# Kernel tuning notes

Hardware: AMD Instinct MI355X
Metric: run time of the kernel (lower is better)

## Reference

```python
import jax, jax.numpy as jnp
import numpy as np

N, K, R = 32768, 4096, 256

def setup_inputs() -> dict:
    key = jax.random.key(0)
    k1, k2, k3 = jax.random.split(key, 3)
    H = jax.random.normal(k1, (N, R), dtype=jnp.float32)
    L = jax.random.normal(k2, (K, R), dtype=jnp.float32)
    W_I = jax.random.normal(k3, (R, R), dtype=jnp.float32)
    return {"H": H, "L": L, "W_I": W_I}

def reference(H, L, W_I):
    # Q = W_I @ L^T : (r, k)
    Q = jnp.einsum('rs,ks->rk', W_I, L)
    # M_I = H @ Q : (n, k)
    M_I = jnp.einsum('nr,rk->nk', H, Q)
    A_I = jax.nn.softmax(M_I, axis=1)
    # C_I = A_I @ L : (n, r)
    C_I = jnp.einsum('nk,kr->nr', A_I, L)
    return (C_I, A_I)
```

## Files before the change

### kernel.cpp

```cpp
#include <hip/hip_runtime.h>
#include <hip/hip_bf16.h>
#include <math.h>
#include <stdint.h>

constexpr int N_ROWS = 32768;
constexpr int K_DIM  = 4096;
constexpr int R_DIM  = 256;
constexpr int KP     = 3 * R_DIM;

typedef __bf16 bf16x8 __attribute__((ext_vector_type(8)));
typedef float  f32x4  __attribute__((ext_vector_type(4)));
typedef unsigned short u16x8 __attribute__((ext_vector_type(8)));
typedef unsigned short u16x4 __attribute__((ext_vector_type(4)));

__device__ __forceinline__ unsigned short f2bf(float x) {
    unsigned u = __float_as_uint(x);
    u += 0x7fffu + ((u >> 16) & 1u);
    return (unsigned short)(u >> 16);
}
__device__ __forceinline__ float bf2f(unsigned short h) {
    return __uint_as_float((unsigned)h << 16);
}

__device__ __forceinline__ void gl2lds16(const void* gptr, void* lptr) {
    __builtin_amdgcn_global_load_lds(
        (const __attribute__((address_space(1))) unsigned int*)gptr,
        (__attribute__((address_space(3))) unsigned int*)lptr,
        16, 0, 0);
}

__global__ __launch_bounds__(256)
void gemm_mfma_nt(const unsigned short* __restrict__ A,
                  const unsigned short* __restrict__ B,
                  float* __restrict__ C, int M, int N, int Kc)
{
    __shared__ __align__(16) unsigned short As[128 * 32];
    __shared__ __align__(16) unsigned short Bs[128 * 32];

    const int tid  = threadIdx.x;
    const int wave = tid >> 6, lane = tid & 63;
    const int wm = wave >> 1, wn = wave & 1;
    const long m0 = (long)blockIdx.x * 128;
    const long n0 = (long)blockIdx.y * 128;

    f32x4 acc[4][4] = {};

    const int srow  = lane >> 2;
    const int skoff = (lane & 3) * 8;
    const int c0 = wave, c1 = wave + 4;
    const int kq = (lane >> 4) * 8;
    const int mr = lane & 15;

    for (int k0 = 0; k0 < Kc; k0 += 32) {
        gl2lds16(A + (m0 + c0 * 16 + srow) * (long)Kc + k0 + skoff, &As[c0 * 512]);
        gl2lds16(A + (m0 + c1 * 16 + srow) * (long)Kc + k0 + skoff, &As[c1 * 512]);
        gl2lds16(B + (n0 + c0 * 16 + srow) * (long)Kc + k0 + skoff, &Bs[c0 * 512]);
        gl2lds16(B + (n0 + c1 * 16 + srow) * (long)Kc + k0 + skoff, &Bs[c1 * 512]);
        __syncthreads();

        bf16x8 af[4], bfr[4];
#pragma unroll
        for (int t = 0; t < 4; ++t) {
            af[t]  = *(const bf16x8*)&As[(wm * 64 + t * 16 + mr) * 32 + kq];
            bfr[t] = *(const bf16x8*)&Bs[(wn * 64 + t * 16 + mr) * 32 + kq];
        }
#pragma unroll
        for (int i = 0; i < 4; ++i)
#pragma unroll
            for (int j = 0; j < 4; ++j)
                acc[i][j] = __builtin_amdgcn_mfma_f32_16x16x32_bf16(
                    af[i], bfr[j], acc[i][j], 0, 0, 0);
        __syncthreads();
    }

    const int col = lane & 15, rquad = (lane >> 4) * 4;
#pragma unroll
    for (int i = 0; i < 4; ++i) {
        const long mrow = m0 + wm * 64 + i * 16 + rquad;
#pragma unroll
        for (int j = 0; j < 4; ++j) {
            float* p = C + mrow * (long)N + n0 + wn * 64 + j * 16 + col;
#pragma unroll
            for (int r = 0; r < 4; ++r) p[(long)r * N] = acc[i][j][r];
        }
    }
}

__global__ __launch_bounds__(512)
void softmax_av(float* __restrict__ Mio,
                const unsigned short* __restrict__ LT,
                float* __restrict__ C)
{
    __shared__ __align__(16) unsigned short Bs[R_DIM * 64];
    __shared__ __align__(16) unsigned short As[64 * 64];
    __shared__ float sm_m[64], sm_inv[64];

    const int tid  = threadIdx.x;
    const int wave = tid >> 6, lane = tid & 63;
    const long m0 = (long)blockIdx.x * 64;

    for (int rr = 0; rr < 8; ++rr) {
        const int row = wave * 8 + rr;
        const float* rp = Mio + (m0 + row) * (long)K_DIM;
        float m = -3.4e38f, s = 0.f;
#pragma unroll
        for (int it = 0; it < 16; ++it) {
            float4 v = ((const float4*)rp)[lane + 64 * it];
            float cm = fmaxf(fmaxf(v.x, v.y), fmaxf(v.z, v.w));
            if (cm > m) { s *= __expf(m - cm); m = cm; }
            s += __expf(v.x - m) + __expf(v.y - m) +
                 __expf(v.z - m) + __expf(v.w - m);
        }
#pragma unroll
        for (int off = 1; off < 64; off <<= 1) {
            float om = __shfl_xor(m, off), os = __shfl_xor(s, off);
            float nm = fmaxf(m, om);
            s = s * __expf(m - nm) + os * __expf(om - nm);
            m = nm;
        }
        if (lane == 0) { sm_m[row] = m; sm_inv[row] = 1.f / s; }
    }
    __syncthreads();

    f32x4 acc[2][4] = {};
    const int wm = wave >> 2, wn = wave & 3;
    const int mr = lane & 15;
    const int kq16 = (lane >> 4) * 16;

    for (int k0 = 0; k0 < K_DIM; k0 += 64) {
#pragma unroll
        for (int q = 0; q < 4; ++q) {
            const int rbase = q * 64 + wave * 8;
            const int rloc  = rbase + (lane >> 3);
            const int phys  = (lane & 7) * 16;
            const int kbyte = phys ^ ((rloc & 7) << 4);
            gl2lds16((const char*)LT + (long)rloc * (K_DIM * 2) + (long)k0 * 2 + kbyte,
                     &Bs[rbase * 64]);
        }
#pragma unroll
        for (int p = 0; p < 2; ++p) {
            const int row = p * 32 + wave * 4 + (lane >> 4);
            const int col = (lane & 15) * 4;
            float* gp = Mio + (m0 + row) * (long)K_DIM + k0 + col;
            float4 v = *(const float4*)gp;
            const float mrow = sm_m[row], inv = sm_inv[row];
            float e0 = __expf(v.x - mrow), e1 = __expf(v.y - mrow);
            float e2 = __expf(v.z - mrow), e3 = __expf(v.w - mrow);
            *(float4*)gp = make_float4(e0 * inv, e1 * inv, e2 * inv, e3 * inv);
            u16x4 u;
            u[0] = f2bf(e0); u[1] = f2bf(e1); u[2] = f2bf(e2); u[3] = f2bf(e3);
            const int byte = (row * 128 + col * 2) ^ ((row & 7) << 4);
            *(u16x4*)((char*)As + byte) = u;
        }
        __syncthreads();

#pragma unroll
        for (int ks = 0; ks < 2; ++ks) {
            bf16x8 af[2], bfr[4];
#pragma unroll
            for (int t = 0; t < 2; ++t) {
                const int arow = wm * 32 + t * 16 + mr;
                const int ab = (arow * 128 + ks * 64 + kq16) ^ ((arow & 7) << 4);
                af[t] = *(const bf16x8*)((const char*)As + ab);
            }
#pragma unroll
            for (int t = 0; t < 4; ++t) {
                const int brow = wn * 64 + t * 16 + mr;
                const int bb = (brow * 128 + ks * 64 + kq16) ^ ((brow & 7) << 4);
                bfr[t] = *(const bf16x8*)((const char*)Bs + bb);
            }
#pragma unroll
            for (int i = 0; i < 2; ++i)
#pragma unroll
                for (int j = 0; j < 4; ++j)
                    acc[i][j] = __builtin_amdgcn_mfma_f32_16x16x32_bf16(
                        af[i], bfr[j], acc[i][j], 0, 0, 0);
        }
        __syncthreads();
    }

    const int col = lane & 15, rquad = (lane >> 4) * 4;
#pragma unroll
    for (int i = 0; i < 2; ++i) {
        const int lrow0 = wm * 32 + i * 16 + rquad;
#pragma unroll
        for (int j = 0; j < 4; ++j) {
            float* p = C + (m0 + lrow0) * (long)R_DIM + wn * 64 + j * 16 + col;
#pragma unroll
            for (int r = 0; r < 4; ++r)
                p[(long)r * R_DIM] = acc[i][j][r] * sm_inv[lrow0 + r];
        }
    }
}

__global__ __launch_bounds__(256)
void prep_B(const float* __restrict__ L, unsigned short* __restrict__ Bp)
{
    const long i = (long)blockIdx.x * 256 + threadIdx.x;
    const long k = i >> 8; const int r = (int)(i & 255);
    const float x = L[i];
    const unsigned short hi = f2bf(x);
    const unsigned short lo = f2bf(x - bf2f(hi));
    unsigned short* row = Bp + k * KP;
    row[r] = hi; row[R_DIM + r] = lo; row[2 * R_DIM + r] = hi;
}

__global__ __launch_bounds__(256)
void prep_LT(const float* __restrict__ L, unsigned short* __restrict__ LT)
{
    const long i = (long)blockIdx.x * 256 + threadIdx.x;
    const long r = i >> 12; const long k = i & 4095;
    LT[r * K_DIM + k] = f2bf(L[k * R_DIM + r]);
}

template<bool BT>
__global__ __launch_bounds__(256)
void gemm128(const float* __restrict__ A, const float* __restrict__ B,
             float* __restrict__ C, int M, int N, int Kc)
{
    __shared__ __align__(16) float Asl[16][132];
    __shared__ __align__(16) float Bsl[16][132];

    const int tid = threadIdx.x;
    const int tx = tid & 15, ty = tid >> 4;
    const long m0 = (long)blockIdx.x * 128;
    const long n0 = (long)blockIdx.y * 128;

    float acc[8][8];
#pragma unroll
    for (int i = 0; i < 8; ++i)
#pragma unroll
        for (int j = 0; j < 8; ++j) acc[i][j] = 0.f;

    for (int k0 = 0; k0 < Kc; k0 += 16) {
#pragma unroll
        for (int q = 0; q < 2; ++q) {
            int fi = tid + 256 * q, row = fi >> 2, col = (fi & 3) * 4;
            float4 v = *(const float4*)(A + (m0 + row) * (long)Kc + k0 + col);
            Asl[col + 0][row] = v.x; Asl[col + 1][row] = v.y;
            Asl[col + 2][row] = v.z; Asl[col + 3][row] = v.w;
        }
        if (BT) {
#pragma unroll
            for (int q = 0; q < 2; ++q) {
                int fi = tid + 256 * q, row = fi >> 2, col = (fi & 3) * 4;
                float4 v = *(const float4*)(B + (n0 + row) * (long)Kc + k0 + col);
                Bsl[col + 0][row] = v.x; Bsl[col + 1][row] = v.y;
                Bsl[col + 2][row] = v.z; Bsl[col + 3][row] = v.w;
            }
        } else {
#pragma unroll
            for (int q = 0; q < 2; ++q) {
                int fi = tid + 256 * q, row = fi >> 5, col = (fi & 31) * 4;
                float4 v = *(const float4*)(B + (k0 + row) * (long)N + n0 + col);
                *(float4*)&Bsl[row][col] = v;
            }
        }
        __syncthreads();
#pragma unroll
        for (int kk = 0; kk < 16; ++kk) {
            float a[8], b[8];
            *(float4*)&a[0] = *(const float4*)&Asl[kk][ty * 8];
            *(float4*)&a[4] = *(const float4*)&Asl[kk][ty * 8 + 4];
            *(float4*)&b[0] = *(const float4*)&Bsl[kk][tx * 8];
            *(float4*)&b[4] = *(const float4*)&Bsl[kk][tx * 8 + 4];
#pragma unroll
            for (int i = 0; i < 8; ++i)
#pragma unroll
                for (int j = 0; j < 8; ++j)
                    acc[i][j] = fmaf(a[i], b[j], acc[i][j]);
        }
        __syncthreads();
    }
#pragma unroll
    for (int i = 0; i < 8; ++i) {
        float* p = C + (m0 + ty * 8 + i) * (long)N + n0 + tx * 8;
        *(float4*)p       = make_float4(acc[i][0], acc[i][1], acc[i][2], acc[i][3]);
        *(float4*)(p + 4) = make_float4(acc[i][4], acc[i][5], acc[i][6], acc[i][7]);
    }
}

__global__ __launch_bounds__(256)
void gemm128_hl(const float* __restrict__ A, const float* __restrict__ B,
                unsigned short* __restrict__ Ap, int M, int N, int Kc)
{
    __shared__ __align__(16) float Asl[16][132];
    __shared__ __align__(16) float Bsl[16][132];

    const int tid = threadIdx.x;
    const int tx = tid & 15, ty = tid >> 4;
    const long m0 = (long)blockIdx.x * 128;
    const long n0 = (long)blockIdx.y * 128;

    float acc[8][8];
#pragma unroll
    for (int i = 0; i < 8; ++i)
#pragma unroll
        for (int j = 0; j < 8; ++j) acc[i][j] = 0.f;

    for (int k0 = 0; k0 < Kc; k0 += 16) {
#pragma unroll
        for (int q = 0; q < 2; ++q) {
            int fi = tid + 256 * q, row = fi >> 2, col = (fi & 3) * 4;
            float4 v = *(const float4*)(A + (m0 + row) * (long)Kc + k0 + col);
            Asl[col + 0][row] = v.x; Asl[col + 1][row] = v.y;
            Asl[col + 2][row] = v.z; Asl[col + 3][row] = v.w;
        }
#pragma unroll
        for (int q = 0; q < 2; ++q) {
            int fi = tid + 256 * q, row = fi >> 5, col = (fi & 31) * 4;
            float4 v = *(const float4*)(B + (k0 + row) * (long)N + n0 + col);
            *(float4*)&Bsl[row][col] = v;
        }
        __syncthreads();
#pragma unroll
        for (int kk = 0; kk < 16; ++kk) {
            float a[8], b[8];
            *(float4*)&a[0] = *(const float4*)&Asl[kk][ty * 8];
            *(float4*)&a[4] = *(const float4*)&Asl[kk][ty * 8 + 4];
            *(float4*)&b[0] = *(const float4*)&Bsl[kk][tx * 8];
            *(float4*)&b[4] = *(const float4*)&Bsl[kk][tx * 8 + 4];
#pragma unroll
            for (int i = 0; i < 8; ++i)
#pragma unroll
                for (int j = 0; j < 8; ++j)
                    acc[i][j] = fmaf(a[i], b[j], acc[i][j]);
        }
        __syncthreads();
    }
#pragma unroll
    for (int i = 0; i < 8; ++i) {
        const long row = m0 + ty * 8 + i;
        const int  cb  = (int)n0 + tx * 8;
        u16x8 vh, vl;
#pragma unroll
        for (int j = 0; j < 8; ++j) {
            const float x = acc[i][j];
            const unsigned short hi = f2bf(x);
            vh[j] = hi;
            vl[j] = f2bf(x - bf2f(hi));
        }
        unsigned short* rp = Ap + row * KP;
        *(u16x8*)(rp + cb)             = vh;
        *(u16x8*)(rp + R_DIM + cb)     = vh;
        *(u16x8*)(rp + 2 * R_DIM + cb) = vl;
    }
}

__global__ __launch_bounds__(256)
void softmax_rows(float* __restrict__ Mio)
{
    const long n  = blockIdx.x;
    float* row    = Mio + n * (long)K_DIM;
    const int tid = threadIdx.x;

    float4 v[4];
    float lmax = -3.4e38f;
#pragma unroll
    for (int q = 0; q < 4; ++q) {
        v[q] = ((const float4*)row)[tid + 256 * q];
        lmax = fmaxf(lmax, fmaxf(fmaxf(v[q].x, v[q].y), fmaxf(v[q].z, v[q].w)));
    }
    __shared__ float redmax[4], redsum[4];
#pragma unroll
    for (int off = 32; off > 0; off >>= 1)
        lmax = fmaxf(lmax, __shfl_xor(lmax, off));
    if ((tid & 63) == 0) redmax[tid >> 6] = lmax;
    __syncthreads();
    const float gmax = fmaxf(fmaxf(redmax[0], redmax[1]), fmaxf(redmax[2], redmax[3]));

    float lsum = 0.f;
#pragma unroll
    for (int q = 0; q < 4; ++q) {
        v[q].x = __expf(v[q].x - gmax); v[q].y = __expf(v[q].y - gmax);
        v[q].z = __expf(v[q].z - gmax); v[q].w = __expf(v[q].w - gmax);
        lsum += v[q].x + v[q].y + v[q].z + v[q].w;
    }
#pragma unroll
    for (int off = 32; off > 0; off >>= 1)
        lsum += __shfl_xor(lsum, off);
    if ((tid & 63) == 0) redsum[tid >> 6] = lsum;
    __syncthreads();
    const float inv = 1.f / (redsum[0] + redsum[1] + redsum[2] + redsum[3]);
#pragma unroll
    for (int q = 0; q < 4; ++q) {
        v[q].x *= inv; v[q].y *= inv; v[q].z *= inv; v[q].w *= inv;
        ((float4*)row)[tid + 256 * q] = v[q];
    }
}

extern "C" void kernel_launch(void* const* d_in, const int* in_sizes, int n_in,
                              void* d_out, int out_size, void* d_ws, size_t ws_size,
                              hipStream_t stream)
{
    const float* H  = (const float*)d_in[0];
    const float* L  = (const float*)d_in[1];
    const float* Wi = (const float*)d_in[2];

    float* Cout = (float*)d_out;
    float* Aout = (float*)d_out + (size_t)N_ROWS * R_DIM;

    const size_t szAp = (size_t)N_ROWS * KP * 2;
    const size_t szBp = (size_t)K_DIM * KP * 2;
    const size_t szLT = (size_t)R_DIM * K_DIM * 2;

    if (ws_size >= szAp + szBp + szLT) {
        unsigned short* Ap = (unsigned short*)d_ws;
        unsigned short* Bp = (unsigned short*)((char*)d_ws + szAp);
        unsigned short* LT = (unsigned short*)((char*)d_ws + szAp + szBp);

        gemm128_hl<<<dim3(N_ROWS / 128, R_DIM / 128), 256, 0, stream>>>(
            H, Wi, Ap, N_ROWS, R_DIM, R_DIM);
        prep_B<<<dim3((K_DIM * R_DIM) / 256), 256, 0, stream>>>(L, Bp);
        prep_LT<<<dim3((R_DIM * K_DIM) / 256), 256, 0, stream>>>(L, LT);
        gemm_mfma_nt<<<dim3(N_ROWS / 128, K_DIM / 128), 256, 0, stream>>>(
            Ap, Bp, Aout, N_ROWS, K_DIM, KP);
        softmax_av<<<dim3(N_ROWS / 64), 512, 0, stream>>>(Aout, LT, Cout);
    } else {
        gemm128<false><<<dim3(N_ROWS / 128, R_DIM / 128), 256, 0, stream>>>(
            H, Wi, Cout, N_ROWS, R_DIM, R_DIM);
        gemm128<true><<<dim3(N_ROWS / 128, K_DIM / 128), 256, 0, stream>>>(
            Cout, L, Aout, N_ROWS, K_DIM, R_DIM);
        softmax_rows<<<dim3(N_ROWS), 256, 0, stream>>>(Aout);
        gemm128<false><<<dim3(N_ROWS / 128, R_DIM / 128), 256, 0, stream>>>(
            Aout, L, Cout, N_ROWS, R_DIM, K_DIM);
    }
}
```

Measured before the change: 1.272 ms.

## Fuse partial softmax statistics into logits GEMM epilogue and pipeline softmax-AV

The logits GEMM epilogue now computes per-tile row max and sum-of-exp and writes them to a partials buffer. A small finalize kernel merges these into per-row max and inverse sum. The softmax-AV kernel no longer rereads the full logits matrix to compute statistics. That kernel is restructured to 32-row blocks with 256 threads, double-buffered LDS, and prefetch of the next K-slice overlapped with MFMA work. This removes one full pass over the 512MB logits matrix, at the cost of extra epilogue shuffles, a new launch and partials traffic.

```diff
diff --git a/kernel.cpp b/kernel.cpp
--- a/kernel.cpp
+++ b/kernel.cpp
@@ -7,6 +7,7 @@
 constexpr int K_DIM  = 4096;
 constexpr int R_DIM  = 256;
 constexpr int KP     = 3 * R_DIM;
+constexpr int KB     = K_DIM / 128;
 
 typedef __bf16 bf16x8 __attribute__((ext_vector_type(8)));
 typedef float  f32x4  __attribute__((ext_vector_type(4)));
@@ -32,10 +33,13 @@
 __global__ __launch_bounds__(256)
 void gemm_mfma_nt(const unsigned short* __restrict__ A,
                   const unsigned short* __restrict__ B,
-                  float* __restrict__ C, int M, int N, int Kc)
+                  float* __restrict__ C,
+                  float* __restrict__ Pm, float* __restrict__ Ps,
+                  int M, int N, int Kc)
 {
     __shared__ __align__(16) unsigned short As[128 * 32];
     __shared__ __align__(16) unsigned short Bs[128 * 32];
+    __shared__ float pm_s[128][2], ps_s[128][2];
 
     const int tid  = threadIdx.x;
     const int wave = tid >> 6, lane = tid & 63;
@@ -84,108 +88,156 @@
             for (int r = 0; r < 4; ++r) p[(long)r * N] = acc[i][j][r];
         }
     }
-}
-
-__global__ __launch_bounds__(512)
-void softmax_av(float* __restrict__ Mio,
-                const unsigned short* __restrict__ LT,
-                float* __restrict__ C)
-{
-    __shared__ __align__(16) unsigned short Bs[R_DIM * 64];
-    __shared__ __align__(16) unsigned short As[64 * 64];
-    __shared__ float sm_m[64], sm_inv[64];
+
+#pragma unroll
+    for (int i = 0; i < 4; ++i) {
+#pragma unroll
+        for (int r = 0; r < 4; ++r) {
+            float mx = fmaxf(fmaxf(acc[i][0][r], acc[i][1][r]),
+                             fmaxf(acc[i][2][r], acc[i][3][r]));
+#pragma unroll
+            for (int off = 1; off < 16; off <<= 1)
+                mx = fmaxf(mx, __shfl_xor(mx, off));
+            float sm = 0.f;
+#pragma unroll
+            for (int j = 0; j < 4; ++j) sm += __expf(acc[i][j][r] - mx);
+#pragma unroll
+            for (int off = 1; off < 16; off <<= 1)
+                sm += __shfl_xor(sm, off);
+            if (mr == 0) {
+                const int rw = wm * 64 + i * 16 + rquad + r;
+                pm_s[rw][wn] = mx;
+                ps_s[rw][wn] = sm;
+            }
+        }
+    }
+    __syncthreads();
+    if (tid < 128) {
+        const float ma = pm_s[tid][0], mb = pm_s[tid][1];
+        const float mx = fmaxf(ma, mb);
+        const float s  = ps_s[tid][0] * __expf(ma - mx) +
+                         ps_s[tid][1] * __expf(mb - mx);
+        Pm[(m0 + tid) * KB + blockIdx.y] = mx;
+        Ps[(m0 + tid) * KB + blockIdx.y] = s;
+    }
+}
+
+__global__ __launch_bounds__(256)
+void finalize_ms(const float* __restrict__ Pm, const float* __restrict__ Ps,
+                 float* __restrict__ SMm, float* __restrict__ SMi)
+{
+    const long row = (long)blockIdx.x * 256 + threadIdx.x;
+    const float4* pm = (const float4*)(Pm + row * KB);
+    const float4* ps = (const float4*)(Ps + row * KB);
+    float4 v[8];
+    float mx = -3.4e38f;
+#pragma unroll
+    for (int q = 0; q < 8; ++q) {
+        v[q] = pm[q];
+        mx = fmaxf(mx, fmaxf(fmaxf(v[q].x, v[q].y), fmaxf(v[q].z, v[q].w)));
+    }
+    float s = 0.f;
+#pragma unroll
+    for (int q = 0; q < 8; ++q) {
+        float4 w = ps[q];
+        s += w.x * __expf(v[q].x - mx) + w.y * __expf(v[q].y - mx) +
+             w.z * __expf(v[q].z - mx) + w.w * __expf(v[q].w - mx);
+    }
+    SMm[row] = mx;
+    SMi[row] = 1.f / s;
+}
+
+__global__ __launch_bounds__(256)
+void softmax_av_sp(float* __restrict__ Mio,
+                   const unsigned short* __restrict__ LT,
+                   const float* __restrict__ SMm, const float* __restrict__ SMi,
+                   float* __restrict__ C)
+{
+    __shared__ __align__(16) unsigned short Bs[2][R_DIM * 32];
+    __shared__ __align__(16) unsigned short As[2][32 * 32];
+    __shared__ float sm_m[32], sm_inv[32];
 
     const int tid  = threadIdx.x;
     const int wave = tid >> 6, lane = tid & 63;
-    const long m0 = (long)blockIdx.x * 64;
-
-    for (int rr = 0; rr < 8; ++rr) {
-        const int row = wave * 8 + rr;
-        const float* rp = Mio + (m0 + row) * (long)K_DIM;
-        float m = -3.4e38f, s = 0.f;
-#pragma unroll
-        for (int it = 0; it < 16; ++it) {
-            float4 v = ((const float4*)rp)[lane + 64 * it];
-            float cm = fmaxf(fmaxf(v.x, v.y), fmaxf(v.z, v.w));
-            if (cm > m) { s *= __expf(m - cm); m = cm; }
-            s += __expf(v.x - m) + __expf(v.y - m) +
-                 __expf(v.z - m) + __expf(v.w - m);
-        }
-#pragma unroll
-        for (int off = 1; off < 64; off <<= 1) {
-            float om = __shfl_xor(m, off), os = __shfl_xor(s, off);
-            float nm = fmaxf(m, om);
-            s = s * __expf(m - nm) + os * __expf(om - nm);
-            m = nm;
-        }
-        if (lane == 0) { sm_m[row] = m; sm_inv[row] = 1.f / s; }
-    }
+    const long m0 = (long)blockIdx.x * 32;
+
+    if (tid < 32) { sm_m[tid] = SMm[m0 + tid]; sm_inv[tid] = SMi[m0 + tid]; }
     __syncthreads();
 
+    const int mr   = lane & 15;
+    const int kq16 = (lane >> 4) * 16;
+    const int arow = tid >> 3;
+    const int acol = (tid & 7) * 4;
+    const int abyte = (arow * 64 + (tid & 7) * 8) ^ ((arow & 3) << 4);
+    const float myM = sm_m[arow], myI = sm_inv[arow];
+    float* const arp = Mio + (m0 + arow) * (long)K_DIM + acol;
+
     f32x4 acc[2][4] = {};
-    const int wm = wave >> 2, wn = wave & 3;
-    const int mr = lane & 15;
-    const int kq16 = (lane >> 4) * 16;
-
-    for (int k0 = 0; k0 < K_DIM; k0 += 64) {
+
+    auto stage_B = [&](int buf, int kk0) {
+#pragma unroll
+        for (int w = 0; w < 4; ++w) {
+            const int rloc = wave * 64 + w * 16 + (lane >> 2);
+            const int sb   = ((lane & 3) * 16) ^ ((rloc & 3) << 4);
+            gl2lds16((const char*)LT + (long)rloc * (K_DIM * 2) + (long)kk0 * 2 + sb,
+                     &Bs[buf][(wave * 64 + w * 16) * 32]);
+        }
+    };
+    auto emit_A = [&](int buf, int kk0, float4 v) {
+        const float e0 = __expf(v.x - myM), e1 = __expf(v.y - myM);
+        const float e2 = __expf(v.z - myM), e3 = __expf(v.w - myM);
+        *(float4*)(arp + kk0) = make_float4(e0 * myI, e1 * myI, e2 * myI, e3 * myI);
+        u16x4 u;
+        u[0] = f2bf(e0); u[1] = f2bf(e1); u[2] = f2bf(e2); u[3] = f2bf(e3);
+        *(u16x4*)((char*)As[buf] + abyte) = u;
+    };
+
+    stage_B(0, 0);
+    emit_A(0, 0, *(const float4*)(arp + 0));
+    __syncthreads();
+
+    int cur = 0;
+    for (int t = 0; t < K_DIM / 32; ++t) {
+        const int nxt = cur ^ 1;
+        float4 vn;
+        const bool has_next = (t < K_DIM / 32 - 1);
+        if (has_next) {
+            stage_B(nxt, (t + 1) * 32);
+            vn = *(const float4*)(arp + (t + 1) * 32);
+        }
+
+        bf16x8 af[2], bfr[4];
+#pragma unroll
+        for (int q = 0; q < 2; ++q) {
+            const int ar = q * 16 + mr;
+            af[q] = *(const bf16x8*)((const char*)As[cur] +
+                    ((ar * 64 + kq16) ^ ((ar & 3) << 4)));
+        }
 #pragma unroll
         for (int q = 0; q < 4; ++q) {
-            const int rbase = q * 64 + wave * 8;
-            const int rloc  = rbase + (lane >> 3);
-            const int phys  = (lane & 7) * 16;
-            const int kbyte = phys ^ ((rloc & 7) << 4);
-            gl2lds16((const char*)LT + (long)rloc * (K_DIM * 2) + (long)k0 * 2 + kbyte,
-                     &Bs[rbase * 64]);
-        }
-#pragma unroll
-        for (int p = 0; p < 2; ++p) {
-            const int row = p * 32 + wave * 4 + (lane >> 4);
-            const int col = (lane & 15) * 4;
-            float* gp = Mio + (m0 + row) * (long)K_DIM + k0 + col;
-            float4 v = *(const float4*)gp;
-            const float mrow = sm_m[row], inv = sm_inv[row];
-            float e0 = __expf(v.x - mrow), e1 = __expf(v.y - mrow);
-            float e2 = __expf(v.z - mrow), e3 = __expf(v.w - mrow);
-            *(float4*)gp = make_float4(e0 * inv, e1 * inv, e2 * inv, e3 * inv);
-            u16x4 u;
-            u[0] = f2bf(e0); u[1] = f2bf(e1); u[2] = f2bf(e2); u[3] = f2bf(e3);
-            const int byte = (row * 128 + col * 2) ^ ((row & 7) << 4);
-            *(u16x4*)((char*)As + byte) = u;
-        }
-        __syncthreads();
-
-#pragma unroll
-        for (int ks = 0; ks < 2; ++ks) {
-            bf16x8 af[2], bfr[4];
-#pragma unroll
-            for (int t = 0; t < 2; ++t) {
-                const int arow = wm * 32 + t * 16 + mr;
-                const int ab = (arow * 128 + ks * 64 + kq16) ^ ((arow & 7) << 4);
-                af[t] = *(const bf16x8*)((const char*)As + ab);
-            }
-#pragma unroll
-            for (int t = 0; t < 4; ++t) {
-                const int brow = wn * 64 + t * 16 + mr;
-                const int bb = (brow * 128 + ks * 64 + kq16) ^ ((brow & 7) << 4);
-                bfr[t] = *(const bf16x8*)((const char*)Bs + bb);
-            }
-#pragma unroll
-            for (int i = 0; i < 2; ++i)
-#pragma unroll
-                for (int j = 0; j < 4; ++j)
-                    acc[i][j] = __builtin_amdgcn_mfma_f32_16x16x32_bf16(
-                        af[i], bfr[j], acc[i][j], 0, 0, 0);
-        }
-        __syncthreads();
+            const int br = wave * 64 + q * 16 + mr;
+            bfr[q] = *(const bf16x8*)((const char*)Bs[cur] +
+                     ((br * 64 + kq16) ^ ((br & 3) << 4)));
+        }
+#pragma unroll
+        for (int i = 0; i < 2; ++i)
+#pragma unroll
+            for (int j = 0; j < 4; ++j)
+                acc[i][j] = __builtin_amdgcn_mfma_f32_16x16x32_bf16(
+                    af[i], bfr[j], acc[i][j], 0, 0, 0);
+
+        if (has_next) emit_A(nxt, (t + 1) * 32, vn);
+        __syncthreads();
+        cur = nxt;
     }
 
     const int col = lane & 15, rquad = (lane >> 4) * 4;
 #pragma unroll
     for (int i = 0; i < 2; ++i) {
-        const int lrow0 = wm * 32 + i * 16 + rquad;
+        const int lrow0 = i * 16 + rquad;
 #pragma unroll
         for (int j = 0; j < 4; ++j) {
-            float* p = C + (m0 + lrow0) * (long)R_DIM + wn * 64 + j * 16 + col;
+            float* p = C + (m0 + lrow0) * (long)R_DIM + wave * 64 + j * 16 + col;
 #pragma unroll
             for (int r = 0; r < 4; ++r)
                 p[(long)r * R_DIM] = acc[i][j][r] * sm_inv[lrow0 + r];
@@ -403,19 +455,29 @@
     const size_t szAp = (size_t)N_ROWS * KP * 2;
     const size_t szBp = (size_t)K_DIM * KP * 2;
     const size_t szLT = (size_t)R_DIM * K_DIM * 2;
-
-    if (ws_size >= szAp + szBp + szLT) {
-        unsigned short* Ap = (unsigned short*)d_ws;
-        unsigned short* Bp = (unsigned short*)((char*)d_ws + szAp);
-        unsigned short* LT = (unsigned short*)((char*)d_ws + szAp + szBp);
+    const size_t szPm = (size_t)N_ROWS * KB * 4;
+    const size_t szPs = (size_t)N_ROWS * KB * 4;
+    const size_t szSM = (size_t)N_ROWS * 4;
+
+    if (ws_size >= szAp + szBp + szLT + szPm + szPs + 2 * szSM) {
+        char* w = (char*)d_ws;
+        unsigned short* Ap = (unsigned short*)w;                 w += szAp;
+        unsigned short* Bp = (unsigned short*)w;                 w += szBp;
+        unsigned short* LT = (unsigned short*)w;                 w += szLT;
+        float* Pm  = (float*)w;                                  w += szPm;
+        float* Ps  = (float*)w;                                  w += szPs;
+        float* SMm = (float*)w;                                  w += szSM;
+        float* SMi = (float*)w;
 
         gemm128_hl<<<dim3(N_ROWS / 128, R_DIM / 128), 256, 0, stream>>>(
             H, Wi, Ap, N_ROWS, R_DIM, R_DIM);
         prep_B<<<dim3((K_DIM * R_DIM) / 256), 256, 0, stream>>>(L, Bp);
         prep_LT<<<dim3((R_DIM * K_DIM) / 256), 256, 0, stream>>>(L, LT);
         gemm_mfma_nt<<<dim3(N_ROWS / 128, K_DIM / 128), 256, 0, stream>>>(
-            Ap, Bp, Aout, N_ROWS, K_DIM, KP);
-        softmax_av<<<dim3(N_ROWS / 64), 512, 0, stream>>>(Aout, LT, Cout);
+            Ap, Bp, Aout, Pm, Ps, N_ROWS, K_DIM, KP);
+        finalize_ms<<<dim3(N_ROWS / 256), 256, 0, stream>>>(Pm, Ps, SMm, SMi);
+        softmax_av_sp<<<dim3(N_ROWS / 32), 256, 0, stream>>>(
+            Aout, LT, SMm, SMi, Cout);
     } else {
         gemm128<false><<<dim3(N_ROWS / 128, R_DIM / 128), 256, 0, stream>>>(
             H, Wi, Cout, N_ROWS, R_DIM, R_DIM);
```

Measured after the change: 1.359 ms. 1.07x slower.
